# Optimization experiments

Measured on AMD Instinct MI355X. Metric: run time of the kernel, lower is better.

The kernel has to match this reference:

```python
import jax, jax.numpy as jnp
import numpy as np

KNN, D, CONV_NUM, LEVELS, POOL_RATIO = 4, 64, 6, 3, 8
QN, RFN, NS, H, W = 4, 32, 4, 64, 64
CN = LEVELS * CONV_NUM  # 18 = 3 embed levels x 6 correlation variants


def instance_norm(x, eps=1e-5):
    # InstanceNorm2d(affine=False): normalize each (sample, channel) over H,W (biased var)
    m = x.mean(axis=(-2, -1), keepdims=True)
    v = x.var(axis=(-2, -1), keepdims=True)
    return (x - m) * jax.lax.rsqrt(v + eps)


def conv2d(x, w, b):
    y = jax.lax.conv_general_dilated(x, w, (1, 1), 'SAME', dimension_numbers=('NCHW', 'OIHW', 'NCHW'))
    return y + b[None, :, None, None]


def conv1x1x1(x, w, b):
    # Conv3d kernel 1x1x1 == pure channel mixing; x: (qn,C,ns,h,w), w: (Cout,Cin)
    return jnp.einsum('qcshw,oc->qoshw', x, w) + b[None, :, None, None, None]


def head(x, w1, b1, w2, b2, w3, b3):
    x = jax.nn.relu(conv2d(x, w1, b1))
    x = jax.nn.relu(conv2d(x, w2, b2))
    return conv2d(x, w3, b3)


def setup_inputs():
    key = jax.random.key(0)
    ks = iter(jax.random.split(key, 64))
    def rn(shape, scale=0.05):
        return jax.random.normal(next(ks), shape, jnp.float32) * scale
    inp = {'corr': jax.random.normal(next(ks), (QN, RFN, NS, CN, H, W), jnp.float32)}
    inp['scale_conv_w1'] = rn((D, CN * KNN)); inp['scale_conv_b1'] = rn((D,))
    inp['scale_conv_w2'] = rn((D, D)); inp['scale_conv_b2'] = rn((D,))
    inp['score_conv_w1'] = rn((D, LEVELS * KNN)); inp['score_conv_b1'] = rn((D,))
    inp['score_conv_w2'] = rn((D, D)); inp['score_conv_b2'] = rn((D,))
    for name, cout in (('scale_pred', 1), ('offset_pred', 2), ('score_pred', 1)):
        inp[name + '_w1'] = rn((D, D, 3, 3)); inp[name + '_b1'] = rn((D,))
        inp[name + '_w2'] = rn((D, D, 3, 3)); inp[name + '_b2'] = rn((D,))
        inp[name + '_w3'] = rn((cout, D, 3, 3)); inp[name + '_b3'] = rn((cout,))
    return inp


def _maps(corr, scale_conv_w1, scale_conv_b1, scale_conv_w2, scale_conv_b2,
          score_conv_w1, score_conv_b1, score_conv_w2, score_conv_b2,
          scale_pred_w1, scale_pred_b1, scale_pred_w2, scale_pred_b2, scale_pred_w3, scale_pred_b3,
          offset_pred_w1, offset_pred_b1, offset_pred_w2, offset_pred_b2, offset_pred_w3, offset_pred_b3,
          score_pred_w1, score_pred_b1, score_pred_w2, score_pred_b2, score_pred_w3, score_pred_b3):
    qn, rfn, ns, cn, h, w = corr.shape
    corr_n = instance_norm(corr)                         # score_norm
    # per-(scale,position) matching score per reference -> knn refs
    ref_score = corr_n.mean(axis=3)                      # qn,rfn,ns,h,w
    rs = jnp.moveaxis(ref_score, 1, -1)                  # qn,ns,h,w,rfn
    _, top_idx = jax.lax.top_k(rs, KNN)                  # qn,ns,h,w,knn
    feat = jnp.transpose(corr_n, (0, 2, 4, 5, 1, 3))     # qn,ns,h,w,rfn,cn
    knn_feat = jnp.take_along_axis(feat, top_idx[..., None], axis=4)  # qn,ns,h,w,knn,cn
    x_scale = jnp.transpose(knn_feat.reshape(qn, ns, h, w, KNN * cn), (0, 4, 1, 2, 3))  # qn,72,ns,h,w
    lvl = corr_n.reshape(qn, rfn, ns, LEVELS, CONV_NUM, h, w).mean(axis=4)  # per-level score
    lvl = jnp.transpose(lvl, (0, 2, 4, 5, 1, 3))         # qn,ns,h,w,rfn,3
    knn_lvl = jnp.take_along_axis(lvl, top_idx[..., None], axis=4)
    x_score = jnp.transpose(knn_lvl.reshape(qn, ns, h, w, KNN * LEVELS), (0, 4, 1, 2, 3))  # qn,12,ns,h,w
    xs = conv1x1x1(jax.nn.relu(conv1x1x1(x_scale, scale_conv_w1, scale_conv_b1)), scale_conv_w2, scale_conv_b2).max(axis=2)
    xc = conv1x1x1(jax.nn.relu(conv1x1x1(x_score, score_conv_w1, score_conv_b1)), score_conv_w2, score_conv_b2).max(axis=2)
    scales = head(xs, scale_pred_w1, scale_pred_b1, scale_pred_w2, scale_pred_b2, scale_pred_w3, scale_pred_b3)
    offsets = head(xc, offset_pred_w1, offset_pred_b1, offset_pred_w2, offset_pred_b2, offset_pred_w3, offset_pred_b3)
    scores = head(xc, score_pred_w1, score_pred_b1, score_pred_w2, score_pred_b2, score_pred_w3, score_pred_b3)
    return scores, scales, offsets


def reference(corr, scale_conv_w1, scale_conv_b1, scale_conv_w2, scale_conv_b2,
              score_conv_w1, score_conv_b1, score_conv_w2, score_conv_b2,
              scale_pred_w1, scale_pred_b1, scale_pred_w2, scale_pred_b2, scale_pred_w3, scale_pred_b3,
              offset_pred_w1, offset_pred_b1, offset_pred_w2, offset_pred_b2, offset_pred_w3, offset_pred_b3,
              score_pred_w1, score_pred_b1, score_pred_w2, score_pred_b2, score_pred_w3, score_pred_b3):
    scores, scales, offsets = _maps(corr, scale_conv_w1, scale_conv_b1, scale_conv_w2, scale_conv_b2,
                                    score_conv_w1, score_conv_b1, score_conv_w2, score_conv_b2,
                                    scale_pred_w1, scale_pred_b1, scale_pred_w2, scale_pred_b2, scale_pred_w3, scale_pred_b3,
                                    offset_pred_w1, offset_pred_b1, offset_pred_w2, offset_pred_b2, offset_pred_w3, offset_pred_b3,
                                    score_pred_w1, score_pred_b1, score_pred_w2, score_pred_b2, score_pred_w3, score_pred_b3)
    # parse_detection: argmax + advanced-index gathers
    qn = scores.shape[0]; h, w = scores.shape[-2:]
    sid = jnp.argmax(scores.reshape(qn, -1), axis=1)
    sy, sx = sid // w, sid % w
    q = jnp.arange(qn)
    off = offsets[q, :, sy, sx]                          # qn,2
    pos = (jnp.stack([sx, sy], -1).astype(scores.dtype) + off + 0.5) * POOL_RATIO - 0.5
    scl = 2.0 ** scales[q, 0, sy, sx]
    return pos, scl, scores, scales, offsets
```

## Files before the change

### kernel.cpp

```cpp
#include <hip/hip_runtime.h>

#define HW 4096

__global__ __launch_bounds__(256) void k_stats_wx(
    const float* __restrict__ corr, float* __restrict__ scl,
    float* __restrict__ shf,
    const float* __restrict__ p0, const float* __restrict__ p1,
    const float* __restrict__ p2, const float* __restrict__ p3,
    const float* __restrict__ p4, const float* __restrict__ p5,
    float* __restrict__ wT, const float* __restrict__ w1s,
    const float* __restrict__ w2s, const float* __restrict__ w1c,
    const float* __restrict__ w2c, float* __restrict__ wm) {
  int t = threadIdx.x;
  if (blockIdx.x < 9216) {
    int g = blockIdx.x;
    const float4* p = (const float4*)(corr + (size_t)g * HW);
    float s = 0.f, s2 = 0.f;
#pragma unroll
    for (int i = 0; i < 4; i++) {
      float4 v = p[t + i * 256];
      s += v.x + v.y + v.z + v.w;
      s2 += v.x * v.x + v.y * v.y + v.z * v.z + v.w * v.w;
    }
#pragma unroll
    for (int o = 32; o > 0; o >>= 1) {
      s += __shfl_down(s, o, 64);
      s2 += __shfl_down(s2, o, 64);
    }
    __shared__ float ls[4], ls2[4];
    int wid = t >> 6;
    if ((t & 63) == 0) { ls[wid] = s; ls2[wid] = s2; }
    __syncthreads();
    if (t == 0) {
      float S = ls[0] + ls[1] + ls[2] + ls[3];
      float S2 = ls2[0] + ls2[1] + ls2[2] + ls2[3];
      float m = S * (1.f / HW);
      float var = S2 * (1.f / HW) - m * m;
      float r = rsqrtf(var + 1e-5f);
      scl[g] = r;
      shf[g] = -m * r;
    }
    return;
  }
  int b = blockIdx.x - 9216;
  if (b < 96) {
    int arr = b >> 4;
    int chunk = b & 15;
    const float* src = (arr == 0) ? p0
                       : (arr == 1) ? p1
                       : (arr == 2) ? p2
                       : (arr == 3) ? p3
                       : (arr == 4) ? p4 : p5;
    float* dst = wT + arr * 36864;
#pragma unroll
    for (int i = 0; i < 9; i++) {
      int e = chunk * 2304 + i * 256 + t;
      int oc = e / 576;
      int rem = e - oc * 576;
      dst[rem * 64 + oc] = src[e];
    }
  } else {
    int i = (b - 96) * 256 + t;
    if (i < 4608) {
      int c = i >> 6, o = i & 63;
      wm[i] = w1s[o * 72 + c];
    } else if (i < 8704) {
      int j = i - 4608;
      int c = j >> 6, o = j & 63;
      wm[i] = w2s[o * 64 + c];
    } else if (i < 9472) {
      int j = i - 8704;
      int c = j >> 6, o = j & 63;
      wm[i] = w1c[o * 12 + c];
    } else if (i < 13568) {
      int j = i - 9472;
      int c = j >> 6, o = j & 63;
      wm[i] = w2c[o * 64 + c];
    }
  }
}

__global__ __launch_bounds__(256) void k_refscore(const float* __restrict__ corr,
                                                  const float* __restrict__ scl,
                                                  const float* __restrict__ shf,
                                                  float* __restrict__ rs) {
  int b = blockIdx.x;
  int grp = b >> 2;
  int i4 = (b & 3) * 256 + threadIdx.x;
  const float* base = corr + (size_t)grp * 18 * HW;
  float4 acc = make_float4(0.f, 0.f, 0.f, 0.f);
  float sh = 0.f;
#pragma unroll
  for (int c = 0; c < 18; c++) {
    float s = scl[grp * 18 + c];
    sh += shf[grp * 18 + c];
    float4 v = ((const float4*)(base + c * HW))[i4];
    acc.x += v.x * s; acc.y += v.y * s; acc.z += v.z * s; acc.w += v.w * s;
  }
  const float inv = 1.f / 18.f;
  float4 o;
  o.x = (acc.x + sh) * inv; o.y = (acc.y + sh) * inv;
  o.z = (acc.z + sh) * inv; o.w = (acc.w + sh) * inv;
  ((float4*)(rs + (size_t)grp * HW))[i4] = o;
}

__global__ __launch_bounds__(256) void k_topk(const float* __restrict__ rs,
                                              int* __restrict__ topidx) {
  __shared__ float st[32 * 256];
  int b = blockIdx.x;
  int pxc = b & 15;
  int ns = (b >> 4) & 3;
  int q = b >> 6;
  int t = threadIdx.x;
  int pxb = pxc * 256;
#pragma unroll 8
  for (int r = 0; r < 32; r++)
    st[r * 256 + t] = rs[((q * 32 + r) * 4 + ns) * HW + pxb + t];
  __syncthreads();
  float v[32];
#pragma unroll
  for (int r = 0; r < 32; r++) v[r] = st[r * 256 + t];
  unsigned mask = 0;
  int sel[4];
#pragma unroll
  for (int k = 0; k < 4; k++) {
    float best = -3.4e38f;
    int bi = 0;
#pragma unroll
    for (int r = 0; r < 32; r++) {
      bool take = (!(mask & (1u << r))) && (v[r] > best);
      best = take ? v[r] : best;
      bi = take ? r : bi;
    }
    sel[k] = bi;
    mask |= (1u << bi);
  }
  ((int4*)topidx)[(q * 4 + ns) * HW + pxb + t] =
      make_int4(sel[0], sel[1], sel[2], sel[3]);
}

__global__ __launch_bounds__(256) void k_gather(const float* __restrict__ corr,
                                                const float* __restrict__ scl,
                                                const float* __restrict__ shf,
                                                const int* __restrict__ topidx,
                                                float* __restrict__ vbuf) {
  __shared__ float ls[32], lsh[32];
  int b = blockIdx.x;
  int c = b % 18;
  int rest = b / 18;
  int ns = rest & 3;
  int pxc = (rest >> 2) & 15;
  int q = rest >> 6;
  int t = threadIdx.x;
  int px = pxc * 256 + t;

  if (t < 32) {
    int g = q * 2304 + t * 72 + ns * 18 + c;
    ls[t] = scl[g];
    lsh[t] = shf[g];
  }
  int4 ti = ((const int4*)topidx)[(q * 4 + ns) * HW + px];
  int rk0 = ti.x, rk1 = ti.y, rk2 = ti.z, rk3 = ti.w;
  __syncthreads();

  const float* base = corr + (size_t)(((q * 32) * 4 + ns) * 18 + c) * HW + px;
  float v0 = 0.f, v1 = 0.f, v2 = 0.f, v3 = 0.f;
#pragma unroll
  for (int r = 0; r < 32; r++) {
    float x = base[(size_t)r * 72 * HW];
    v0 = (rk0 == r) ? x : v0;
    v1 = (rk1 == r) ? x : v1;
    v2 = (rk2 == r) ? x : v2;
    v3 = (rk3 == r) ? x : v3;
  }
  v0 = v0 * ls[rk0] + lsh[rk0];
  v1 = v1 * ls[rk1] + lsh[rk1];
  v2 = v2 * ls[rk2] + lsh[rk2];
  v3 = v3 * ls[rk3] + lsh[rk3];
  size_t ob = (size_t)((q * 4 + ns) * 72 + c) * HW + px;
  vbuf[ob] = v0;
  vbuf[ob + 18 * HW] = v1;
  vbuf[ob + 36 * HW] = v2;
  vbuf[ob + 54 * HW] = v3;
}

#define NSMAX_STORE(OUTP)                                     \
  _Pragma("unroll") for (int og = 0; og < 8; og++) {          \
    _Pragma("unroll") for (int j = 0; j < 8; j++)             \
        red8[j * 256 + t] = a[og * 8 + j];                    \
    __syncthreads();                                          \
    _Pragma("unroll") for (int jj = 0; jj < 2; jj++) {        \
      int j2 = ns * 2 + jj;                                   \
      float m = red8[j2 * 256 + lane];                        \
      _Pragma("unroll") for (int n2 = 1; n2 < 4; n2++)        \
          m = fmaxf(m, red8[j2 * 256 + n2 * 64 + lane]);      \
      OUTP[(size_t)(q * 64 + og * 8 + j2) * HW + px] = m;     \
    }                                                         \
    __syncthreads();                                          \
  }

__global__ __launch_bounds__(256, 2) void k_mlpf(
    const float* __restrict__ vbuf, const float* __restrict__ wm,
    const float* __restrict__ b1s, const float* __restrict__ b2s,
    const float* __restrict__ b1c, const float* __restrict__ b2c,
    float* __restrict__ xs, float* __restrict__ xc) {
  __shared__ float red8[8 * 256];
  int blk = blockIdx.x;
  int q = blk >> 6, pxc = blk & 63;
  int t = threadIdx.x;
  int ns = t >> 6;
  int lane = t & 63;
  int px = pxc * 64 + lane;

  const float* vb = vbuf + (size_t)((q * 4 + ns) * 72) * HW + px;

  float h[64];
#pragma unroll
  for (int o = 0; o < 64; o++) h[o] = b1s[o];
  float xsc[12];
#pragma unroll
  for (int l = 0; l < 12; l++) xsc[l] = 0.f;
#pragma unroll
  for (int c0 = 0; c0 < 72; c0 += 8) {
    float x[8];
#pragma unroll
    for (int j = 0; j < 8; j++) x[j] = vb[(size_t)(c0 + j) * HW];
#pragma unroll
    for (int j = 0; j < 8; j++) {
      const float* wr = wm + (c0 + j) * 64;
#pragma unroll
      for (int o = 0; o < 64; o++) h[o] = fmaf(wr[o], x[j], h[o]);
    }
#pragma unroll
    for (int j = 0; j < 8; j++) xsc[(c0 + j) / 6] += x[j];
  }
#pragma unroll
  for (int o = 0; o < 64; o++) h[o] = fmaxf(h[o], 0.f);
  float a[64];
#pragma unroll
  for (int o = 0; o < 64; o++) a[o] = b2s[o];
#pragma unroll
  for (int c = 0; c < 64; c++) {
    const float* wr = wm + 4608 + c * 64;
    float x = h[c];
#pragma unroll
    for (int o = 0; o < 64; o++) a[o] = fmaf(wr[o], x, a[o]);
  }
  NSMAX_STORE(xs)

#pragma unroll
  for (int l = 0; l < 12; l++) xsc[l] *= (1.f / 6.f);
#pragma unroll
  for (int o = 0; o < 64; o++) h[o] = b1c[o];
#pragma unroll
  for (int c = 0; c < 12; c++) {
    const float* wr = wm + 8704 + c * 64;
    float x = xsc[c];
#pragma unroll
    for (int o = 0; o < 64; o++) h[o] = fmaf(wr[o], x, h[o]);
  }
#pragma unroll
  for (int o = 0; o < 64; o++) h[o] = fmaxf(h[o], 0.f);
#pragma unroll
  for (int o = 0; o < 64; o++) a[o] = b2c[o];
#pragma unroll
  for (int c = 0; c < 64; c++) {
    const float* wr = wm + 9472 + c * 64;
    float x = h[c];
#pragma unroll
    for (int o = 0; o < 64; o++) a[o] = fmaf(wr[o], x, a[o]);
  }
  NSMAX_STORE(xc)
}

template <bool RELU>
__global__ __launch_bounds__(256) void k_conv3h(
    const float* __restrict__ in0, const float* __restrict__ in1,
    const float* __restrict__ in2, const float* __restrict__ w0,
    const float* __restrict__ w1, const float* __restrict__ w2,
    const float* __restrict__ bb0, const float* __restrict__ bb1,
    const float* __restrict__ bb2, float* __restrict__ o0,
    float* __restrict__ o1, float* __restrict__ o2) {
  __shared__ float tile[16 * 10 * 72];
  int b = blockIdx.x;
  int hi = b >> 5;
  int og = hi / 3;
  int head = hi - og * 3;
  int q = (b >> 3) & 3;
  int rt = b & 7;
  const float* in = head == 0 ? in0 : head == 1 ? in1 : in2;
  const float* wT = head == 0 ? w0 : head == 1 ? w1 : w2;
  const float* bb = head == 0 ? bb0 : head == 1 ? bb1 : bb2;
  float* outp = head == 0 ? o0 : head == 1 ? o1 : o2;

  int t = threadIdx.x;
  int w = t & 63;
  int wr = t >> 6;
  int lane4 = t & 15;
  int rgrp = t >> 4;
  float acc[2][16];
#pragma unroll
  for (int pr = 0; pr < 2; pr++)
#pragma unroll
    for (int o = 0; o < 16; o++) acc[pr][o] = 0.f;
  const float* inq = in + (size_t)q * 64 * HW;

  for (int icc = 0; icc < 4; icc++) {
    __syncthreads();
    if (t < 160) { tile[t * 72 + 3] = 0.f; tile[t * 72 + 68] = 0.f; }
#pragma unroll
    for (int p = 0; p < 10; p++) {
      int idx = p * 16 + rgrp;
      int ch = idx / 10;
      int r = idx - ch * 10;
      int grow = rt * 8 + r - 1;
      float4 val = make_float4(0.f, 0.f, 0.f, 0.f);
      if (grow >= 0 && grow < 64)
        val = *(const float4*)(inq + (size_t)(icc * 16 + ch) * HW + grow * 64 +
                               lane4 * 4);
      *(float4*)(tile + idx * 72 + 4 + lane4 * 4) = val;
    }
    __syncthreads();
#pragma unroll 2
    for (int ic = 0; ic < 16; ic++) {
      float xv[4][3];
      const float* tb = tile + (ic * 10 + wr * 2) * 72 + w + 3;
#pragma unroll
      for (int rr = 0; rr < 4; rr++)
#pragma unroll
        for (int dc = 0; dc < 3; dc++) xv[rr][dc] = tb[rr * 72 + dc];
      const float* wb = wT + (size_t)(icc * 16 + ic) * 9 * 64 + og * 16;
#pragma unroll
      for (int dr = 0; dr < 3; dr++)
#pragma unroll
        for (int dc = 0; dc < 3; dc++) {
          const float* wv = wb + (dr * 3 + dc) * 64;
#pragma unroll
          for (int o = 0; o < 16; o++) {
            float wj = wv[o];
            acc[0][o] = fmaf(wj, xv[0 + dr][dc], acc[0][o]);
            acc[1][o] = fmaf(wj, xv[1 + dr][dc], acc[1][o]);
          }
        }
    }
  }
#pragma unroll
  for (int pr = 0; pr < 2; pr++) {
    int orow = rt * 8 + wr * 2 + pr;
#pragma unroll
    for (int o = 0; o < 16; o++) {
      float rz = acc[pr][o] + bb[og * 16 + o];
      if (RELU) rz = fmaxf(rz, 0.f);
      outp[((size_t)q * 64 + og * 16 + o) * HW + orow * 64 + w] = rz;
    }
  }
}

__global__ __launch_bounds__(256) void k_convSh(
    const float* __restrict__ in0, const float* __restrict__ in1,
    const float* __restrict__ in2, const float* __restrict__ wt0,
    const float* __restrict__ wt1, const float* __restrict__ wt2,
    const float* __restrict__ bb0, const float* __restrict__ bb1,
    const float* __restrict__ bb2, float* __restrict__ o0,
    float* __restrict__ o1, float* __restrict__ o2) {
  __shared__ float tile[64 * 3 * 66];
  __shared__ float red[4 * 2 * 64];
  int b = blockIdx.x;
  int head = b >> 8;
  int q = (b >> 6) & 3;
  int row = b & 63;
  const float* in = head == 0 ? in0 : head == 1 ? in1 : in2;
  const float* wt = head == 0 ? wt0 : head == 1 ? wt1 : wt2;
  const float* bb = head == 0 ? bb0 : head == 1 ? bb1 : bb2;
  float* outp = head == 0 ? o0 : head == 1 ? o1 : o2;
  int noc = (head == 1) ? 2 : 1;

  int t = threadIdx.x;
  int w = t & 63;
  int sub = t >> 6;
  if (t < 192) { tile[t * 66] = 0.f; tile[t * 66 + 65] = 0.f; }
  __syncthreads();
  const float* inq = in + (size_t)q * 64 * HW;
#pragma unroll
  for (int i = 0; i < 48; i++) {
    int idx = i * 4 + sub;
    int ic = idx / 3;
    int r = idx - ic * 3;
    int grow = row + r - 1;
    float val = 0.f;
    if (grow >= 0 && grow < 64) val = inq[(size_t)ic * HW + grow * 64 + w];
    tile[idx * 66 + 1 + w] = val;
  }
  __syncthreads();
  float acc0 = 0.f, acc1 = 0.f;
#pragma unroll 4
  for (int i = 0; i < 16; i++) {
    int ic = sub * 16 + i;
    float x[9];
#pragma unroll
    for (int dr = 0; dr < 3; dr++)
#pragma unroll
      for (int dc = 0; dc < 3; dc++)
        x[dr * 3 + dc] = tile[(ic * 3 + dr) * 66 + w + dc];
    const float* wb = wt + (size_t)ic * 9;
#pragma unroll
    for (int j = 0; j < 9; j++) acc0 += wb[j] * x[j];
    if (noc == 2) {
      const float* wb1 = wt + 576 + (size_t)ic * 9;
#pragma unroll
      for (int j = 0; j < 9; j++) acc1 += wb1[j] * x[j];
    }
  }
  red[(sub * 2 + 0) * 64 + w] = acc0;
  if (noc == 2) red[(sub * 2 + 1) * 64 + w] = acc1;
  __syncthreads();
  if (t < 128) {
    int o = t >> 6;
    if (o < noc) {
      float s = red[(0 * 2 + o) * 64 + w] + red[(1 * 2 + o) * 64 + w] +
                red[(2 * 2 + o) * 64 + w] + red[(3 * 2 + o) * 64 + w] + bb[o];
      outp[((size_t)q * noc + o) * HW + row * 64 + w] = s;
    }
  }
}

__global__ __launch_bounds__(256) void k_final(const float* __restrict__ scores,
                                               const float* __restrict__ scales,
                                               const float* __restrict__ offsets,
                                               float* __restrict__ pos,
                                               float* __restrict__ sclo) {
  int q = blockIdx.x, t = threadIdx.x;
  float best = -3.4e38f;
  int bi = 1 << 30;
  for (int i = t; i < HW; i += 256) {
    float v = scores[q * HW + i];
    if (v > best) { best = v; bi = i; }
  }
  __shared__ float bv[256];
  __shared__ int bix[256];
  bv[t] = best;
  bix[t] = bi;
  __syncthreads();
  for (int s = 128; s > 0; s >>= 1) {
    if (t < s) {
      if (bv[t + s] > bv[t] || (bv[t + s] == bv[t] && bix[t + s] < bix[t])) {
        bv[t] = bv[t + s];
        bix[t] = bix[t + s];
      }
    }
    __syncthreads();
  }
  if (t == 0) {
    int sid = bix[0];
    int sy = sid >> 6, sx = sid & 63;
    float o0 = offsets[(q * 2 + 0) * HW + sid];
    float o1 = offsets[(q * 2 + 1) * HW + sid];
    pos[q * 2 + 0] = ((float)sx + o0 + 0.5f) * 8.f - 0.5f;
    pos[q * 2 + 1] = ((float)sy + o1 + 0.5f) * 8.f - 0.5f;
    sclo[q] = exp2f(scales[q * HW + sid]);
  }
}

extern "C" void kernel_launch(void* const* d_in, const int* in_sizes, int n_in,
                              void* d_out, int out_size, void* d_ws, size_t ws_size,
                              hipStream_t stream) {
  const float* corr = (const float*)d_in[0];
  const float* w1s = (const float*)d_in[1];
  const float* b1s = (const float*)d_in[2];
  const float* w2s = (const float*)d_in[3];
  const float* b2s = (const float*)d_in[4];
  const float* w1c = (const float*)d_in[5];
  const float* b1c = (const float*)d_in[6];
  const float* w2c = (const float*)d_in[7];
  const float* b2c = (const float*)d_in[8];

  float* out = (float*)d_out;
  float* pos = out;
  float* sclo = out + 8;
  float* scores = out + 12;
  float* scales = out + 12 + 16384;
  float* offsets = out + 12 + 32768;

  char* ws = (char*)d_ws;
  float* st_scl = (float*)(ws + 0);
  float* st_shf = (float*)(ws + 36864);
  int* topidx = (int*)(ws + 73728);
  float* rs = (float*)(ws + 1122304);
  float* vbuf = rs;
  float* wT = (float*)(ws + 19996672);
  float* wmT = (float*)(ws + 20881408);
  float* xs = (float*)(ws + 20971520);
  float* xc = (float*)(ws + 25165824);
  float* t1s = vbuf;
  float* t1o = (float*)((char*)vbuf + 4194304);
  float* t1c = (float*)((char*)vbuf + 8388608);
  float* t2c = (float*)((char*)vbuf + 12582912);
  float* t2s = xs;
  float* t2o = xc;

  k_stats_wx<<<9365, 256, 0, stream>>>(
      corr, st_scl, st_shf, (const float*)d_in[9], (const float*)d_in[11],
      (const float*)d_in[15], (const float*)d_in[17], (const float*)d_in[21],
      (const float*)d_in[23], wT, w1s, w2s, w1c, w2c, wmT);
  k_refscore<<<2048, 256, 0, stream>>>(corr, st_scl, st_shf, rs);
  k_topk<<<256, 256, 0, stream>>>(rs, topidx);
  k_gather<<<4608, 256, 0, stream>>>(corr, st_scl, st_shf, topidx, vbuf);
  k_mlpf<<<256, 256, 0, stream>>>(vbuf, wmT, b1s, b2s, b1c, b2c, xs, xc);
  k_conv3h<true><<<384, 256, 0, stream>>>(
      xs, xc, xc, wT, wT + 2 * 36864, wT + 4 * 36864,
      (const float*)d_in[10], (const float*)d_in[16], (const float*)d_in[22],
      t1s, t1o, t1c);
  k_conv3h<true><<<384, 256, 0, stream>>>(
      t1s, t1o, t1c, wT + 1 * 36864, wT + 3 * 36864, wT + 5 * 36864,
      (const float*)d_in[12], (const float*)d_in[18], (const float*)d_in[24],
      t2s, t2o, t2c);
  k_convSh<<<768, 256, 0, stream>>>(
      t2s, t2o, t2c, (const float*)d_in[13], (const float*)d_in[19],
      (const float*)d_in[25], (const float*)d_in[14], (const float*)d_in[20],
      (const float*)d_in[26], scales, offsets, scores);

  k_final<<<4, 256, 0, stream>>>(scores, scales, offsets, pos, sclo);
}
```

Measured before the change: 652.9 us.

## Fuse instance-norm stats with reference score and rework MLP into LDS-tiled blocks

The separate stats and refscore kernels are merged so that each block reduces all 18 channels of one group and then rereads that group's data, which is likely cache-resident, to write the normalized mean score. This saves a kernel launch and part of a global pass over corr, but launches only 512 large blocks with 36 per-thread accumulators. The per-pixel MLP kernel is also restructured: inputs and hidden activations are staged in LDS, each thread computes a 16-output slice instead of all 64, and the max over ns is taken from LDS. That cuts register pressure and raises the block count from 256 to 1024, at the cost of more LDS traffic and barriers.

```diff
diff --git a/kernel.cpp b/kernel.cpp
--- a/kernel.cpp
+++ b/kernel.cpp
@@ -2,9 +2,9 @@
 
 #define HW 4096
 
-__global__ __launch_bounds__(256) void k_stats_wx(
+__global__ __launch_bounds__(256) void k_statsrs(
     const float* __restrict__ corr, float* __restrict__ scl,
-    float* __restrict__ shf,
+    float* __restrict__ shf, float* __restrict__ rs,
     const float* __restrict__ p0, const float* __restrict__ p1,
     const float* __restrict__ p2, const float* __restrict__ p3,
     const float* __restrict__ p4, const float* __restrict__ p5,
@@ -12,96 +12,119 @@
     const float* __restrict__ w2s, const float* __restrict__ w1c,
     const float* __restrict__ w2c, float* __restrict__ wm) {
   int t = threadIdx.x;
-  if (blockIdx.x < 9216) {
-    int g = blockIdx.x;
-    const float4* p = (const float4*)(corr + (size_t)g * HW);
-    float s = 0.f, s2 = 0.f;
+  if (blockIdx.x >= 512) {
+    int b = blockIdx.x - 512;
+    if (b < 96) {
+      int arr = b >> 4;
+      int chunk = b & 15;
+      const float* src = (arr == 0) ? p0
+                         : (arr == 1) ? p1
+                         : (arr == 2) ? p2
+                         : (arr == 3) ? p3
+                         : (arr == 4) ? p4 : p5;
+      float* dst = wT + arr * 36864;
+#pragma unroll
+      for (int i = 0; i < 9; i++) {
+        int e = chunk * 2304 + i * 256 + t;
+        int oc = e / 576;
+        int rem = e - oc * 576;
+        dst[rem * 64 + oc] = src[e];
+      }
+    } else {
+      int i = (b - 96) * 256 + t;
+      if (i < 4608) {
+        int c = i >> 6, o = i & 63;
+        wm[i] = w1s[o * 72 + c];
+      } else if (i < 8704) {
+        int j = i - 4608;
+        int c = j >> 6, o = j & 63;
+        wm[i] = w2s[o * 64 + c];
+      } else if (i < 9472) {
+        int j = i - 8704;
+        int c = j >> 6, o = j & 63;
+        wm[i] = w1c[o * 12 + c];
+      } else if (i < 13568) {
+        int j = i - 9472;
+        int c = j >> 6, o = j & 63;
+        wm[i] = w2c[o * 64 + c];
+      }
+    }
+    return;
+  }
+  int g = blockIdx.x;
+  const float4* p = (const float4*)(corr + (size_t)g * 18 * HW);
+
+  float s[18], s2[18];
+#pragma unroll
+  for (int c = 0; c < 18; c++) { s[c] = 0.f; s2[c] = 0.f; }
+#pragma unroll
+  for (int c = 0; c < 18; c++) {
 #pragma unroll
     for (int i = 0; i < 4; i++) {
-      float4 v = p[t + i * 256];
-      s += v.x + v.y + v.z + v.w;
-      s2 += v.x * v.x + v.y * v.y + v.z * v.z + v.w * v.w;
-    }
-#pragma unroll
-    for (int o = 32; o > 0; o >>= 1) {
-      s += __shfl_down(s, o, 64);
-      s2 += __shfl_down(s2, o, 64);
-    }
-    __shared__ float ls[4], ls2[4];
-    int wid = t >> 6;
-    if ((t & 63) == 0) { ls[wid] = s; ls2[wid] = s2; }
-    __syncthreads();
-    if (t == 0) {
-      float S = ls[0] + ls[1] + ls[2] + ls[3];
-      float S2 = ls2[0] + ls2[1] + ls2[2] + ls2[3];
-      float m = S * (1.f / HW);
-      float var = S2 * (1.f / HW) - m * m;
-      float r = rsqrtf(var + 1e-5f);
-      scl[g] = r;
-      shf[g] = -m * r;
-    }
-    return;
-  }
-  int b = blockIdx.x - 9216;
-  if (b < 96) {
-    int arr = b >> 4;
-    int chunk = b & 15;
-    const float* src = (arr == 0) ? p0
-                       : (arr == 1) ? p1
-                       : (arr == 2) ? p2
-                       : (arr == 3) ? p3
-                       : (arr == 4) ? p4 : p5;
-    float* dst = wT + arr * 36864;
-#pragma unroll
-    for (int i = 0; i < 9; i++) {
-      int e = chunk * 2304 + i * 256 + t;
-      int oc = e / 576;
-      int rem = e - oc * 576;
-      dst[rem * 64 + oc] = src[e];
-    }
-  } else {
-    int i = (b - 96) * 256 + t;
-    if (i < 4608) {
-      int c = i >> 6, o = i & 63;
-      wm[i] = w1s[o * 72 + c];
-    } else if (i < 8704) {
-      int j = i - 4608;
-      int c = j >> 6, o = j & 63;
-      wm[i] = w2s[o * 64 + c];
-    } else if (i < 9472) {
-      int j = i - 8704;
-      int c = j >> 6, o = j & 63;
-      wm[i] = w1c[o * 12 + c];
-    } else if (i < 13568) {
-      int j = i - 9472;
-      int c = j >> 6, o = j & 63;
-      wm[i] = w2c[o * 64 + c];
-    }
-  }
-}
-
-__global__ __launch_bounds__(256) void k_refscore(const float* __restrict__ corr,
-                                                  const float* __restrict__ scl,
-                                                  const float* __restrict__ shf,
-                                                  float* __restrict__ rs) {
-  int b = blockIdx.x;
-  int grp = b >> 2;
-  int i4 = (b & 3) * 256 + threadIdx.x;
-  const float* base = corr + (size_t)grp * 18 * HW;
-  float4 acc = make_float4(0.f, 0.f, 0.f, 0.f);
-  float sh = 0.f;
+      float4 v = p[(c << 10) + (i << 8) + t];
+      s[c] += v.x + v.y + v.z + v.w;
+      s2[c] += v.x * v.x + v.y * v.y + v.z * v.z + v.w * v.w;
+    }
+  }
 #pragma unroll
   for (int c = 0; c < 18; c++) {
-    float s = scl[grp * 18 + c];
-    sh += shf[grp * 18 + c];
-    float4 v = ((const float4*)(base + c * HW))[i4];
-    acc.x += v.x * s; acc.y += v.y * s; acc.z += v.z * s; acc.w += v.w * s;
-  }
+#pragma unroll
+    for (int o = 1; o < 64; o <<= 1) {
+      s[c] += __shfl_xor(s[c], o, 64);
+      s2[c] += __shfl_xor(s2[c], o, 64);
+    }
+  }
+  __shared__ float lds_s[4][18], lds_s2[4][18];
+  __shared__ float lds_scl[18], lds_shf[18];
+  int wid = t >> 6;
+  int ln = t & 63;
+  if (ln < 18) {
+    float vs = 0.f, vs2 = 0.f;
+#pragma unroll
+    for (int c = 0; c < 18; c++) {
+      vs = (ln == c) ? s[c] : vs;
+      vs2 = (ln == c) ? s2[c] : vs2;
+    }
+    lds_s[wid][ln] = vs;
+    lds_s2[wid][ln] = vs2;
+  }
+  __syncthreads();
+  if (t < 18) {
+    float S = lds_s[0][t] + lds_s[1][t] + lds_s[2][t] + lds_s[3][t];
+    float S2 = lds_s2[0][t] + lds_s2[1][t] + lds_s2[2][t] + lds_s2[3][t];
+    float m = S * (1.f / HW);
+    float var = S2 * (1.f / HW) - m * m;
+    float r = rsqrtf(var + 1e-5f);
+    scl[g * 18 + t] = r;
+    shf[g * 18 + t] = -m * r;
+    lds_scl[t] = r;
+    lds_shf[t] = -m * r;
+  }
+  __syncthreads();
+
+  float shsum = 0.f;
+#pragma unroll
+  for (int c = 0; c < 18; c++) shsum += lds_shf[c];
   const float inv = 1.f / 18.f;
-  float4 o;
-  o.x = (acc.x + sh) * inv; o.y = (acc.y + sh) * inv;
-  o.z = (acc.z + sh) * inv; o.w = (acc.w + sh) * inv;
-  ((float4*)(rs + (size_t)grp * HW))[i4] = o;
+#pragma unroll
+  for (int i = 0; i < 4; i++) {
+    float4 acc = make_float4(0.f, 0.f, 0.f, 0.f);
+#pragma unroll
+    for (int c = 0; c < 18; c++) {
+      float4 v = p[(c << 10) + (i << 8) + t];
+      float sc = lds_scl[c];
+      acc.x = fmaf(v.x, sc, acc.x);
+      acc.y = fmaf(v.y, sc, acc.y);
+      acc.z = fmaf(v.z, sc, acc.z);
+      acc.w = fmaf(v.w, sc, acc.w);
+    }
+    float4 o;
+    o.x = (acc.x + shsum) * inv;
+    o.y = (acc.y + shsum) * inv;
+    o.z = (acc.z + shsum) * inv;
+    o.w = (acc.w + shsum) * inv;
+    ((float4*)(rs + (size_t)g * HW))[(i << 8) + t] = o;
+  }
 }
 
 __global__ __launch_bounds__(256) void k_topk(const float* __restrict__ rs,
@@ -184,93 +207,122 @@
   vbuf[ob + 54 * HW] = v3;
 }
 
-#define NSMAX_STORE(OUTP)                                     \
-  _Pragma("unroll") for (int og = 0; og < 8; og++) {          \
-    _Pragma("unroll") for (int j = 0; j < 8; j++)             \
-        red8[j * 256 + t] = a[og * 8 + j];                    \
-    __syncthreads();                                          \
-    _Pragma("unroll") for (int jj = 0; jj < 2; jj++) {        \
-      int j2 = ns * 2 + jj;                                   \
-      float m = red8[j2 * 256 + lane];                        \
-      _Pragma("unroll") for (int n2 = 1; n2 < 4; n2++)        \
-          m = fmaxf(m, red8[j2 * 256 + n2 * 64 + lane]);      \
-      OUTP[(size_t)(q * 64 + og * 8 + j2) * HW + px] = m;     \
-    }                                                         \
-    __syncthreads();                                          \
-  }
-
-__global__ __launch_bounds__(256, 2) void k_mlpf(
+__global__ __launch_bounds__(256, 4) void k_mlp2(
     const float* __restrict__ vbuf, const float* __restrict__ wm,
     const float* __restrict__ b1s, const float* __restrict__ b2s,
     const float* __restrict__ b1c, const float* __restrict__ b2c,
     float* __restrict__ xs, float* __restrict__ xc) {
-  __shared__ float red8[8 * 256];
+  __shared__ float lx[72 * 64];
+  __shared__ float lh[64 * 64];
+  __shared__ float lxsc[12 * 64];
   int blk = blockIdx.x;
-  int q = blk >> 6, pxc = blk & 63;
+  int q = blk >> 8, pxg = blk & 255;
   int t = threadIdx.x;
-  int ns = t >> 6;
-  int lane = t & 63;
-  int px = pxc * 64 + lane;
-
-  const float* vb = vbuf + (size_t)((q * 4 + ns) * 72) * HW + px;
-
-  float h[64];
-#pragma unroll
-  for (int o = 0; o < 64; o++) h[o] = b1s[o];
-  float xsc[12];
-#pragma unroll
-  for (int l = 0; l < 12; l++) xsc[l] = 0.f;
-#pragma unroll
-  for (int c0 = 0; c0 < 72; c0 += 8) {
-    float x[8];
-#pragma unroll
-    for (int j = 0; j < 8; j++) x[j] = vb[(size_t)(c0 + j) * HW];
-#pragma unroll
-    for (int j = 0; j < 8; j++) {
-      const float* wr = wm + (c0 + j) * 64;
-#pragma unroll
-      for (int o = 0; o < 64; o++) h[o] = fmaf(wr[o], x[j], h[o]);
-    }
-#pragma unroll
-    for (int j = 0; j < 8; j++) xsc[(c0 + j) / 6] += x[j];
-  }
-#pragma unroll
-  for (int o = 0; o < 64; o++) h[o] = fmaxf(h[o], 0.f);
-  float a[64];
-#pragma unroll
-  for (int o = 0; o < 64; o++) a[o] = b2s[o];
+  int wi = t & 63;
+  int oseg = t >> 6;
+  int px0 = pxg * 16;
+
+  const float* vq = vbuf + (size_t)(q * 4) * 72 * HW + px0;
+#pragma unroll
+  for (int j = 0; j < 18; j++) {
+    int e = j * 256 + t;
+    int c = e >> 6;
+    int w2 = e & 63;
+    int nns = w2 >> 4, ppx = w2 & 15;
+    lx[c * 64 + w2] = vq[(size_t)(nns * 72 + c) * HW + ppx];
+  }
+  __syncthreads();
+
+#pragma unroll
+  for (int m = 0; m < 3; m++) {
+    int idx = m * 256 + t;
+    int l = idx >> 6, w2 = idx & 63;
+    float sm = 0.f;
+#pragma unroll
+    for (int j = 0; j < 6; j++) sm += lx[(l * 6 + j) * 64 + w2];
+    lxsc[l * 64 + w2] = sm * (1.f / 6.f);
+  }
+
+  float h[16];
+  const float* bp1 = b1s + oseg * 16;
+#pragma unroll
+  for (int o = 0; o < 16; o++) h[o] = bp1[o];
+#pragma unroll
+  for (int c = 0; c < 72; c++) {
+    float x = lx[c * 64 + wi];
+    const float* wr = wm + c * 64 + oseg * 16;
+#pragma unroll
+    for (int o = 0; o < 16; o++) h[o] = fmaf(wr[o], x, h[o]);
+  }
+#pragma unroll
+  for (int o = 0; o < 16; o++) lh[(oseg * 16 + o) * 64 + wi] = fmaxf(h[o], 0.f);
+  __syncthreads();
+
+  float a[16];
+  const float* bp2 = b2s + oseg * 16;
+#pragma unroll
+  for (int o = 0; o < 16; o++) a[o] = bp2[o];
 #pragma unroll
   for (int c = 0; c < 64; c++) {
-    const float* wr = wm + 4608 + c * 64;
-    float x = h[c];
-#pragma unroll
-    for (int o = 0; o < 64; o++) a[o] = fmaf(wr[o], x, a[o]);
-  }
-  NSMAX_STORE(xs)
-
-#pragma unroll
-  for (int l = 0; l < 12; l++) xsc[l] *= (1.f / 6.f);
-#pragma unroll
-  for (int o = 0; o < 64; o++) h[o] = b1c[o];
+    float x = lh[c * 64 + wi];
+    const float* wr = wm + 4608 + c * 64 + oseg * 16;
+#pragma unroll
+    for (int o = 0; o < 16; o++) a[o] = fmaf(wr[o], x, a[o]);
+  }
+#pragma unroll
+  for (int o = 0; o < 16; o++) lx[(oseg * 16 + o) * 64 + wi] = a[o];
+  __syncthreads();
+
+#pragma unroll
+  for (int m = 0; m < 4; m++) {
+    int idx = m * 256 + t;
+    int oc = idx >> 4, ppx = idx & 15;
+    float v = lx[oc * 64 + ppx];
+    v = fmaxf(v, lx[oc * 64 + 16 + ppx]);
+    v = fmaxf(v, lx[oc * 64 + 32 + ppx]);
+    v = fmaxf(v, lx[oc * 64 + 48 + ppx]);
+    xs[(size_t)(q * 64 + oc) * HW + px0 + ppx] = v;
+  }
+
+  const float* bc1 = b1c + oseg * 16;
+#pragma unroll
+  for (int o = 0; o < 16; o++) h[o] = bc1[o];
 #pragma unroll
   for (int c = 0; c < 12; c++) {
-    const float* wr = wm + 8704 + c * 64;
-    float x = xsc[c];
-#pragma unroll
-    for (int o = 0; o < 64; o++) h[o] = fmaf(wr[o], x, h[o]);
-  }
-#pragma unroll
-  for (int o = 0; o < 64; o++) h[o] = fmaxf(h[o], 0.f);
-#pragma unroll
-  for (int o = 0; o < 64; o++) a[o] = b2c[o];
+    float x = lxsc[c * 64 + wi];
+    const float* wr = wm + 8704 + c * 64 + oseg * 16;
+#pragma unroll
+    for (int o = 0; o < 16; o++) h[o] = fmaf(wr[o], x, h[o]);
+  }
+  __syncthreads();
+#pragma unroll
+  for (int o = 0; o < 16; o++) lh[(oseg * 16 + o) * 64 + wi] = fmaxf(h[o], 0.f);
+  __syncthreads();
+
+  const float* bc2 = b2c + oseg * 16;
+#pragma unroll
+  for (int o = 0; o < 16; o++) a[o] = bc2[o];
 #pragma unroll
   for (int c = 0; c < 64; c++) {
-    const float* wr = wm + 9472 + c * 64;
-    float x = h[c];
-#pragma unroll
-    for (int o = 0; o < 64; o++) a[o] = fmaf(wr[o], x, a[o]);
-  }
-  NSMAX_STORE(xc)
+    float x = lh[c * 64 + wi];
+    const float* wr = wm + 9472 + c * 64 + oseg * 16;
+#pragma unroll
+    for (int o = 0; o < 16; o++) a[o] = fmaf(wr[o], x, a[o]);
+  }
+#pragma unroll
+  for (int o = 0; o < 16; o++) lx[(oseg * 16 + o) * 64 + wi] = a[o];
+  __syncthreads();
+
+#pragma unroll
+  for (int m = 0; m < 4; m++) {
+    int idx = m * 256 + t;
+    int oc = idx >> 4, ppx = idx & 15;
+    float v = lx[oc * 64 + ppx];
+    v = fmaxf(v, lx[oc * 64 + 16 + ppx]);
+    v = fmaxf(v, lx[oc * 64 + 32 + ppx]);
+    v = fmaxf(v, lx[oc * 64 + 48 + ppx]);
+    xc[(size_t)(q * 64 + oc) * HW + px0 + ppx] = v;
+  }
 }
 
 template <bool RELU>
@@ -498,14 +550,13 @@
   float* t2s = xs;
   float* t2o = xc;
 
-  k_stats_wx<<<9365, 256, 0, stream>>>(
-      corr, st_scl, st_shf, (const float*)d_in[9], (const float*)d_in[11],
+  k_statsrs<<<661, 256, 0, stream>>>(
+      corr, st_scl, st_shf, rs, (const float*)d_in[9], (const float*)d_in[11],
       (const float*)d_in[15], (const float*)d_in[17], (const float*)d_in[21],
       (const float*)d_in[23], wT, w1s, w2s, w1c, w2c, wmT);
-  k_refscore<<<2048, 256, 0, stream>>>(corr, st_scl, st_shf, rs);
   k_topk<<<256, 256, 0, stream>>>(rs, topidx);
   k_gather<<<4608, 256, 0, stream>>>(corr, st_scl, st_shf, topidx, vbuf);
-  k_mlpf<<<256, 256, 0, stream>>>(vbuf, wmT, b1s, b2s, b1c, b2c, xs, xc);
+  k_mlp2<<<1024, 256, 0, stream>>>(vbuf, wmT, b1s, b2s, b1c, b2c, xs, xc);
   k_conv3h<true><<<384, 256, 0, stream>>>(
       xs, xc, xc, wT, wT + 2 * 36864, wT + 4 * 36864,
       (const float*)d_in[10], (const float*)d_in[16], (const float*)d_in[22],
```

Result: faster. 600.5 us (-8.0%).
